# Performance work log

Measured on AMD Instinct MI355X. Metric: run time of the kernel, lower is better.

Reference implementation:

```python
import jax, jax.numpy as jnp
import numpy as np

B, P, D = 256, 256, 514          # batch, num_patches (16^2), model_dim
H, HD = 8, 64                    # n_heads, head_dim ((D-2)//H)
SH = 256                         # shared_hidden = head_mlp_hidden_dims[0]
HH = 256                         # per-head hidden (head_mlp_hidden_dims[1])
DFF = 2048                       # ffn hidden
LH = 2 * SH                      # lat_modulator hidden = shared_hidden*2
LD = D - 2                       # learnable_dim

def gelu(x):
    return jax.nn.gelu(x, approximate=False)  # torch nn.GELU default is exact erf

def setup_inputs() -> dict:
    key = jax.random.key(0)
    ks = jax.random.split(key, 16)
    s = 0.02
    x = jax.random.normal(ks[0], (B, P, D), dtype=jnp.float32)
    # shared spatial layer: Linear(P -> SH), torch weight layout [out, in]
    Ws = jax.random.normal(ks[1], (SH, P), dtype=jnp.float32) * s
    bs = jax.random.normal(ks[2], (SH,), dtype=jnp.float32) * s
    # lat modulator: Linear(2 -> LH), GELU, Linear(LH -> 2*SH) with special init
    LW1 = jax.random.normal(ks[3], (LH, 2), dtype=jnp.float32) * s
    Lb1 = jax.random.normal(ks[4], (LH,), dtype=jnp.float32) * s
    LW2 = jnp.zeros((2 * SH, LH), dtype=jnp.float32)  # zeroed per module init
    Lb2 = jnp.concatenate([jnp.ones((SH,), jnp.float32), jnp.zeros((SH,), jnp.float32)])
    # per-head processing: Linear(SH->HH), GELU, Linear(HH->P), stacked over heads
    HW1 = jax.random.normal(ks[5], (H, HH, SH), dtype=jnp.float32) * s
    Hb1 = jax.random.normal(ks[6], (H, HH), dtype=jnp.float32) * s
    HW2 = jax.random.normal(ks[7], (H, P, HH), dtype=jnp.float32) * s
    Hb2 = jax.random.normal(ks[8], (H, P), dtype=jnp.float32) * s
    # ffn: Linear(D -> DFF) with last-2 input cols zeroed, GELU, Linear(DFF -> LD)
    FW1 = jax.random.normal(ks[9], (DFF, D), dtype=jnp.float32) * s
    FW1 = FW1.at[:, -2:].set(0.0)
    Fb1 = jax.random.normal(ks[10], (DFF,), dtype=jnp.float32) * s
    FW2 = jax.random.normal(ks[11], (LD, DFF), dtype=jnp.float32) * s
    Fb2 = jax.random.normal(ks[12], (LD,), dtype=jnp.float32) * s
    return dict(x=x, Ws=Ws, bs=bs, LW1=LW1, Lb1=Lb1, LW2=LW2, Lb2=Lb2,
                HW1=HW1, Hb1=Hb1, HW2=HW2, Hb2=Hb2,
                FW1=FW1, Fb1=Fb1, FW2=FW2, Fb2=Fb2)

def reference(x, Ws, bs, LW1, Lb1, LW2, Lb2, HW1, Hb1, HW2, Hb2, FW1, Fb1, FW2, Fb2):
    central = P // 2
    sc_central = x[:, central, -2:]          # [B, 2]
    sc_all = x[:, :, -2:]                    # [B, P, 2]
    x_learn = x[:, :, :-2]                   # [B, P, LD]
    x_res = x_learn
    # all heads at once: [B, P, H, HD] -> [B, H, HD, P]
    xh = x_learn.reshape(B, P, H, HD).transpose(0, 2, 3, 1)
    shared = jnp.einsum('bhdp,op->bhdo', xh, Ws) + bs   # [B, H, HD, SH]
    # FiLM params (loop-invariant in original, hoisted here)
    mod = gelu(sc_central @ LW1.T + Lb1) @ LW2.T + Lb2  # [B, 2*SH]
    gamma = mod[:, :SH][:, None, None, :]
    beta = mod[:, SH:][:, None, None, :]
    shared = shared * gamma + beta
    # per-head MLPs as grouped GEMMs
    h = gelu(jnp.einsum('bhdo,hko->bhdk', shared, HW1) + Hb1[None, :, None, :])
    out = jnp.einsum('bhdk,hpk->bhdp', h, HW2) + Hb2[None, :, None, :]  # [B,H,HD,P]
    x_learn = out.transpose(0, 3, 1, 2).reshape(B, P, LD) + x_res
    x_full = jnp.concatenate([x_learn, sc_all], axis=-1)  # [B, P, D]
    f = gelu(x_full @ FW1.T + Fb1) @ FW2.T + Fb2          # [B, P, LD]
    x_learn = f + x_learn
    return jnp.concatenate([x_learn, sc_all], axis=-1)
```

## Files before the change

kernel.cpp:

```cpp
#include <hip/hip_runtime.h>
#include <math.h>

typedef __attribute__((ext_vector_type(8))) __bf16 bf16x8;
typedef __attribute__((ext_vector_type(4))) float f32x4;
typedef __attribute__((ext_vector_type(2))) float f32x2;

#define DEV __device__ __forceinline__

typedef __attribute__((address_space(3))) unsigned int lds_u32;
typedef __attribute__((address_space(1))) unsigned int glb_u32;

DEV unsigned short f2bf(float f) {
    unsigned int u = __builtin_bit_cast(unsigned int, f);
    u += 0x7FFFu + ((u >> 16) & 1u);
    return (unsigned short)(u >> 16);
}
DEV float bf2f(unsigned short u) {
    unsigned int v = (unsigned int)u << 16;
    return __builtin_bit_cast(float, v);
}
DEV unsigned int pack2(float a, float b) {
    return (unsigned int)f2bf(a) | ((unsigned int)f2bf(b) << 16);
}
DEV float gelu_exact(float v) {
    return 0.5f * v * (1.0f + erff(v * 0.70710678118654752f));
}
DEV float gelu_fast(float x) {
    float z = 1.5957691216f * x + 0.0713548163f * x * x * x;
    float e = __expf(-z);
    return x * __builtin_amdgcn_rcpf(1.0f + e);
}

__global__ void cast_bf16_kernel(const float* __restrict__ src,
                                 unsigned short* __restrict__ dst, int n) {
    int i = blockIdx.x * 256 + threadIdx.x;
    if (i < n) dst[i] = f2bf(src[i]);
}

__global__ void cast_fw1_kernel(const float* __restrict__ src,
                                unsigned short* __restrict__ dst) {
    int i = blockIdx.x * 256 + threadIdx.x;
    if (i < 2048 * 512) {
        int row = i >> 9, k = i & 511;
        dst[i] = f2bf(src[row * 514 + k]);
    }
}

__global__ void gb_kernel(const float* __restrict__ x,
                          const float* __restrict__ LW1, const float* __restrict__ Lb1,
                          const float* __restrict__ LW2, const float* __restrict__ Lb2,
                          float* __restrict__ gb) {
    __shared__ float t[8][512];
    const int b0 = blockIdx.x * 8, tid = threadIdx.x;
    for (int idx = tid; idx < 8 * 512; idx += 256) {
        int bb = idx >> 9, j = idx & 511;
        float s0 = x[((size_t)(b0 + bb) * 256 + 128) * 514 + 512];
        float s1 = x[((size_t)(b0 + bb) * 256 + 128) * 514 + 513];
        t[bb][j] = gelu_exact(LW1[j * 2] * s0 + LW1[j * 2 + 1] * s1 + Lb1[j]);
    }
    __syncthreads();
    const int i = tid;
    float a0[8], a1[8];
    float l0 = Lb2[i], l1 = Lb2[i + 256];
    #pragma unroll
    for (int bb = 0; bb < 8; ++bb) { a0[bb] = l0; a1[bb] = l1; }
    for (int j = 0; j < 512; ++j) {
        float w0 = LW2[(size_t)i * 512 + j];
        float w1 = LW2[(size_t)(i + 256) * 512 + j];
        #pragma unroll
        for (int bb = 0; bb < 8; ++bb) {
            a0[bb] += w0 * t[bb][j];
            a1[bb] += w1 * t[bb][j];
        }
    }
    #pragma unroll
    for (int bb = 0; bb < 8; ++bb) {
        gb[(size_t)(b0 + bb) * 512 + i] = a0[bb];
        gb[(size_t)(b0 + bb) * 512 + i + 256] = a1[bb];
    }
}

__global__ void sc_copy_kernel(const float* __restrict__ x, float* __restrict__ out,
                               float* __restrict__ scbuf) {
    size_t idx = (size_t)blockIdx.x * 256 + threadIdx.x;
    size_t off = idx * 514 + 512;
    f32x2 v = *(const f32x2*)(x + off);
    *(f32x2*)(out + off) = v;
    *(f32x2*)(scbuf + idx * 2) = v;
}

#define MPAD 264

__global__ __launch_bounds__(256, 2) void mixer_kernel(
    const float* __restrict__ x, const float* __restrict__ bs,
    const float* __restrict__ Hb1, const float* __restrict__ Hb2,
    const unsigned short* __restrict__ Wsb,
    const unsigned short* __restrict__ HW1b,
    const unsigned short* __restrict__ HW2b,
    const float* __restrict__ gb,
    float* __restrict__ out,
    unsigned short* __restrict__ Xb) {
    __shared__ __attribute__((aligned(16))) char smem[33792 + 34816];
    unsigned short* XT = (unsigned short*)smem;
    unsigned short* S = (unsigned short*)(smem + 33792);
    unsigned short* ST = S;

    const int bid = blockIdx.x;
    const int b = bid >> 3;
    const int h = bid & 7;
    const int tid = threadIdx.x;
    const int lane = tid & 63;
    const int w = tid >> 6;
    const int l15 = lane & 15;
    const int l4 = lane >> 4;

    {
        const int c = lane;
        const float* xp = x + ((size_t)b * 256) * 514 + (size_t)h * 64 + c;
        for (int i = 0; i < 32; ++i) {
            int p = (i * 4 + w) * 2;
            float v0 = xp[(size_t)p * 514];
            float v1 = xp[(size_t)(p + 1) * 514];
            *(unsigned int*)&XT[c * MPAD + p] = pack2(v0, v1);
        }
    }
    __syncthreads();

    f32x4 acc[4][4];

    #pragma unroll
    for (int mt = 0; mt < 4; ++mt)
        #pragma unroll
        for (int nt = 0; nt < 4; ++nt) acc[mt][nt] = 0.f;
    {
        bf16x8 bnx[4];
        #pragma unroll
        for (int nt = 0; nt < 4; ++nt)
            bnx[nt] = *(const bf16x8*)(Wsb + (size_t)(w * 64 + nt * 16 + l15) * 256 + l4 * 8);
        for (int kc = 0; kc < 8; ++kc) {
            bf16x8 bcur[4];
            #pragma unroll
            for (int nt = 0; nt < 4; ++nt) bcur[nt] = bnx[nt];
            if (kc < 7) {
                #pragma unroll
                for (int nt = 0; nt < 4; ++nt)
                    bnx[nt] = *(const bf16x8*)(Wsb + (size_t)(w * 64 + nt * 16 + l15) * 256 + (kc + 1) * 32 + l4 * 8);
            }
            #pragma unroll
            for (int mt = 0; mt < 4; ++mt) {
                bf16x8 afr = *(const bf16x8*)&XT[(mt * 16 + l15) * MPAD + kc * 32 + l4 * 8];
                #pragma unroll
                for (int nt = 0; nt < 4; ++nt)
                    acc[mt][nt] = __builtin_amdgcn_mfma_f32_16x16x32_bf16(afr, bcur[nt], acc[mt][nt], 0, 0, 0);
            }
        }
    }
    #pragma unroll
    for (int nt = 0; nt < 4; ++nt) {
        int o = w * 64 + nt * 16 + l15;
        float bsv = bs[o];
        float g = gb[(size_t)b * 512 + o];
        float be = gb[(size_t)b * 512 + 256 + o];
        #pragma unroll
        for (int mt = 0; mt < 4; ++mt)
            #pragma unroll
            for (int r = 0; r < 4; ++r) {
                int c = mt * 16 + l4 * 4 + r;
                S[c * MPAD + o] = f2bf((acc[mt][nt][r] + bsv) * g + be);
            }
    }
    __syncthreads();

    const unsigned short* W2p = HW1b + (size_t)h * 65536;
    #pragma unroll
    for (int mt = 0; mt < 4; ++mt)
        #pragma unroll
        for (int nt = 0; nt < 4; ++nt) acc[mt][nt] = 0.f;
    {
        bf16x8 bnx[4];
        #pragma unroll
        for (int nt = 0; nt < 4; ++nt)
            bnx[nt] = *(const bf16x8*)(W2p + (size_t)(w * 64 + nt * 16 + l15) * 256 + l4 * 8);
        for (int kc = 0; kc < 8; ++kc) {
            bf16x8 bcur[4];
            #pragma unroll
            for (int nt = 0; nt < 4; ++nt) bcur[nt] = bnx[nt];
            if (kc < 7) {
                #pragma unroll
                for (int nt = 0; nt < 4; ++nt)
                    bnx[nt] = *(const bf16x8*)(W2p + (size_t)(w * 64 + nt * 16 + l15) * 256 + (kc + 1) * 32 + l4 * 8);
            }
            #pragma unroll
            for (int mt = 0; mt < 4; ++mt) {
                bf16x8 afr = *(const bf16x8*)&S[(mt * 16 + l15) * MPAD + kc * 32 + l4 * 8];
                #pragma unroll
                for (int nt = 0; nt < 4; ++nt)
                    acc[mt][nt] = __builtin_amdgcn_mfma_f32_16x16x32_bf16(afr, bcur[nt], acc[mt][nt], 0, 0, 0);
            }
        }
    }
    #pragma unroll
    for (int nt = 0; nt < 4; ++nt) {
        int kk = w * 64 + nt * 16 + l15;
        float hb = Hb1[(size_t)h * 256 + kk];
        #pragma unroll
        for (int mt = 0; mt < 4; ++mt)
            #pragma unroll
            for (int r = 0; r < 4; ++r) {
                int c = mt * 16 + l4 * 4 + r;
                XT[c * MPAD + kk] = f2bf(gelu_fast(acc[mt][nt][r] + hb));
            }
    }
    __syncthreads();

    const unsigned short* W3p = HW2b + (size_t)h * 65536;
    #pragma unroll
    for (int mt = 0; mt < 4; ++mt)
        #pragma unroll
        for (int nt = 0; nt < 4; ++nt) acc[mt][nt] = 0.f;
    {
        bf16x8 bnx[4];
        #pragma unroll
        for (int nt = 0; nt < 4; ++nt)
            bnx[nt] = *(const bf16x8*)(W3p + (size_t)(w * 64 + nt * 16 + l15) * 256 + l4 * 8);
        for (int kc = 0; kc < 8; ++kc) {
            bf16x8 bcur[4];
            #pragma unroll
            for (int nt = 0; nt < 4; ++nt) bcur[nt] = bnx[nt];
            if (kc < 7) {
                #pragma unroll
                for (int nt = 0; nt < 4; ++nt)
                    bnx[nt] = *(const bf16x8*)(W3p + (size_t)(w * 64 + nt * 16 + l15) * 256 + (kc + 1) * 32 + l4 * 8);
            }
            #pragma unroll
            for (int mt = 0; mt < 4; ++mt) {
                bf16x8 afr = *(const bf16x8*)&XT[(mt * 16 + l15) * MPAD + kc * 32 + l4 * 8];
                #pragma unroll
                for (int nt = 0; nt < 4; ++nt)
                    acc[mt][nt] = __builtin_amdgcn_mfma_f32_16x16x32_bf16(afr, bcur[nt], acc[mt][nt], 0, 0, 0);
            }
        }
    }
    #pragma unroll
    for (int nt = 0; nt < 4; ++nt) {
        int p = w * 64 + nt * 16 + l15;
        float hb = Hb2[(size_t)h * 256 + p];
        #pragma unroll
        for (int mt = 0; mt < 4; ++mt) {
            ushort4 uv;
            uv.x = f2bf(acc[mt][nt][0] + hb);
            uv.y = f2bf(acc[mt][nt][1] + hb);
            uv.z = f2bf(acc[mt][nt][2] + hb);
            uv.w = f2bf(acc[mt][nt][3] + hb);
            *(ushort4*)(ST + p * 68 + mt * 16 + l4 * 4) = uv;
        }
    }
    __syncthreads();

    #pragma unroll
    for (int s = 0; s < 16; ++s) {
        int row = s * 16 + w * 4 + l4;
        ushort4 u = *(const ushort4*)(ST + row * 68 + l15 * 4);
        const float* xr = x + ((size_t)(b * 256 + row)) * 514 + h * 64 + l15 * 4;
        f32x2 xa = *(const f32x2*)xr;
        f32x2 xc = *(const f32x2*)(xr + 2);
        float o0 = bf2f(u.x) + xa.x;
        float o1 = bf2f(u.y) + xa.y;
        float o2 = bf2f(u.z) + xc.x;
        float o3 = bf2f(u.w) + xc.y;
        float* orow = out + ((size_t)(b * 256 + row)) * 514 + h * 64 + l15 * 4;
        f32x2 w0; w0.x = o0; w0.y = o1;
        f32x2 w1; w1.x = o2; w1.y = o3;
        *(f32x2*)orow = w0;
        *(f32x2*)(orow + 2) = w1;
        ushort4 xo;
        xo.x = f2bf(o0); xo.y = f2bf(o1); xo.z = f2bf(o2); xo.w = f2bf(o3);
        *(ushort4*)(Xb + ((size_t)(b * 256 + row)) * 512 + h * 64 + l15 * 4) = xo;
    }
}

DEV void stage_half(const unsigned short* g, size_t gstride, int row0, int k0,
                    char* half_base, int w, int lane) {
    const int slot = lane & 7;
    const int r8 = lane >> 3;
    const int swz = (slot ^ r8) * 16;
    #pragma unroll
    for (int i = 0; i < 2; ++i) {
        int chunk = w * 2 + i;
        int row = chunk * 8 + r8;
        const char* src = (const char*)(g + (size_t)(row0 + row) * gstride + k0) + swz;
        __builtin_amdgcn_global_load_lds((const glb_u32*)src,
                                         (lds_u32*)(half_base + chunk * 1024), 16, 0, 0);
    }
}

DEV void stage4(const unsigned short* A, size_t sA, int m0,
                const unsigned short* B, size_t sB, int n0, int k0,
                char* Abuf, char* Bbuf, int w, int lane) {
    stage_half(A, sA, m0, k0, Abuf, w, lane);
    stage_half(A, sA, m0 + 128, k0, Abuf + 16384, w, lane);
    stage_half(B, sB, n0, k0, Bbuf, w, lane);
    stage_half(B, sB, n0 + 128, k0, Bbuf + 16384, w, lane);
}

DEV void tile_body(const unsigned short* A, size_t sA, int m0,
                   const unsigned short* B, size_t sB, int n0,
                   char* smem, int cb, int kn, bool more,
                   int vA0, int vA1, int vB0, int vB1,
                   int w, int lane, f32x4 (&acc)[8][4]) {
    if (more) {
        int nb = 32768 - cb;
        stage4(A, sA, m0, B, sB, n0, kn, smem + nb, smem + 65536 + nb, w, lane);
    }
    __builtin_amdgcn_s_setprio(1);
    #pragma unroll
    for (int kk = 0; kk < 2; ++kk) {
        const int vA = kk ? vA1 : vA0;
        const int vB = kk ? vB1 : vB0;
        bf16x8 bf[4];
        #pragma unroll
        for (int nf = 0; nf < 4; ++nf)
            bf[nf] = *(const bf16x8*)(smem + vB + cb + nf * 2048);
        #pragma unroll
        for (int mh = 0; mh < 2; ++mh) {
            bf16x8 af[4];
            #pragma unroll
            for (int mf = 0; mf < 4; ++mf)
                af[mf] = *(const bf16x8*)(smem + vA + cb + mh * 8192 + mf * 2048);
            #pragma unroll
            for (int mf = 0; mf < 4; ++mf)
                #pragma unroll
                for (int nf = 0; nf < 4; ++nf)
                    acc[mh * 4 + mf][nf] = __builtin_amdgcn_mfma_f32_16x16x32_bf16(
                        af[mf], bf[nf], acc[mh * 4 + mf][nf], 0, 0, 0);
        }
    }
    __builtin_amdgcn_s_setprio(0);
    if (more) asm volatile("s_waitcnt vmcnt(0)" ::: "memory");
    __builtin_amdgcn_s_barrier();
}

DEV void gemm_loop(const unsigned short* A, size_t sA,
                   const unsigned short* B, size_t sB,
                   int m0, int n0, int NT,
                   char* smem, int w, int lane, f32x4 (&acc)[8][4]) {
    const int wm = w >> 2, wn = w & 3;
    const int l15 = lane & 15, l4 = lane >> 4;
    const int sw = (l15 & 7) << 4;
    const int k0off = (l4 * 16) ^ sw;
    const int k1off = (64 + l4 * 16) ^ sw;
    const int aBase = (wm * 128 + l15) * 128;
    const int bBase = 65536 + (wn * 64 + l15) * 128;
    const int vA0 = aBase + k0off, vA1 = aBase + k1off;
    const int vB0 = bBase + k0off, vB1 = bBase + k1off;

    stage4(A, sA, m0, B, sB, n0, 0, smem, smem + 65536, w, lane);
    asm volatile("s_waitcnt vmcnt(0)" ::: "memory");
    __builtin_amdgcn_s_barrier();

    for (int t = 0; t < NT; t += 2) {
        tile_body(A, sA, m0, B, sB, n0, smem, 0, (t + 1) * 64, t + 1 < NT,
                  vA0, vA1, vB0, vB1, w, lane, acc);
        tile_body(A, sA, m0, B, sB, n0, smem, 32768, (t + 2) * 64, t + 2 < NT,
                  vA0, vA1, vB0, vB1, w, lane, acc);
    }
}

__global__ __launch_bounds__(512, 1) void gemm1_kernel(
    const unsigned short* __restrict__ A,
    const unsigned short* __restrict__ B,
    const float* __restrict__ Fb1,
    const float* __restrict__ FW1,
    const float* __restrict__ scbuf,
    long pass_m0,
    unsigned short* __restrict__ G) {
    __shared__ __attribute__((aligned(16))) char smem[131072];

    const int nwg = gridDim.x;
    const int cpx = nwg >> 3;
    const int bid = (blockIdx.x & 7) * cpx + (blockIdx.x >> 3);
    const int m0 = (bid >> 3) * 256;
    const int n0 = (bid & 7) * 256;
    const int tid = threadIdx.x;
    const int lane = tid & 63;
    const int w = tid >> 6;
    const int l15 = lane & 15;
    const int l4 = lane >> 4;
    const int wm = w >> 2, wn = w & 3;

    f32x4 acc[8][4];
    #pragma unroll
    for (int mf = 0; mf < 8; ++mf)
        #pragma unroll
        for (int nf = 0; nf < 4; ++nf) acc[mf][nf] = 0.f;

    gemm_loop(A, 512, B, 512, m0, n0, 8, smem, w, lane, acc);

    float fb[4], wa[4], wb[4];
    #pragma unroll
    for (int nf = 0; nf < 4; ++nf) {
        int n = n0 + wn * 64 + nf * 16 + l15;
        fb[nf] = Fb1[n];
        wa[nf] = FW1[(size_t)n * 514 + 512];
        wb[nf] = FW1[(size_t)n * 514 + 513];
    }
    unsigned short* LT = (unsigned short*)smem;
    #pragma unroll
    for (int ph = 0; ph < 2; ++ph) {
        if (wm == ph) {
            #pragma unroll
            for (int mfg = 0; mfg < 8; ++mfg) {
                f32x2 sc[4];
                #pragma unroll
                for (int r = 0; r < 4; ++r) {
                    long rowg = pass_m0 + m0 + ph * 128 + mfg * 16 + l4 * 4 + r;
                    sc[r] = *(const f32x2*)(scbuf + rowg * 2);
                }
                #pragma unroll
                for (int nf = 0; nf < 4; ++nf)
                    #pragma unroll
                    for (int r = 0; r < 4; ++r) {
                        float v = acc[mfg][nf][r] + fb[nf] + sc[r].x * wa[nf] + sc[r].y * wb[nf];
                        int rl = mfg * 16 + l4 * 4 + r;
                        LT[rl * 264 + wn * 64 + nf * 16 + l15] = f2bf(gelu_fast(v));
                    }
            }
        }
        __syncthreads();
        {
            const int row16 = tid >> 5, col16 = tid & 31;
            #pragma unroll
            for (int sp = 0; sp < 8; ++sp) {
                int row = sp * 16 + row16;
                uint4 d = *(const uint4*)((const char*)smem + row * 528 + col16 * 16);
                *(uint4*)(G + ((size_t)(m0 + ph * 128 + row)) * 2048 + n0 + col16 * 8) = d;
            }
        }
        __syncthreads();
    }
}

__global__ __launch_bounds__(512, 1) void gemm2_kernel(
    const unsigned short* __restrict__ A,
    const unsigned short* __restrict__ B,
    const float* __restrict__ Fb2,
    long pass_m0,
    float* __restrict__ io) {
    __shared__ __attribute__((aligned(16))) char smem[131072];

    const int nwg = gridDim.x;
    const int cpx = nwg >> 3;
    const int bid = (blockIdx.x & 7) * cpx + (blockIdx.x >> 3);
    const int m0 = (bid >> 1) * 256;
    const int n0 = (bid & 1) * 256;
    const int tid = threadIdx.x;
    const int lane = tid & 63;
    const int w = tid >> 6;
    const int l15 = lane & 15;
    const int l4 = lane >> 4;
    const int wm = w >> 2, wn = w & 3;

    f32x4 acc[8][4];
    #pragma unroll
    for (int mf = 0; mf < 8; ++mf)
        #pragma unroll
        for (int nf = 0; nf < 4; ++nf) acc[mf][nf] = 0.f;

    gemm_loop(A, 2048, B, 2048, m0, n0, 32, smem, w, lane, acc);

    #pragma unroll
    for (int nf = 0; nf < 4; ++nf) {
        int n = n0 + wn * 64 + nf * 16 + l15;
        float fbv = Fb2[n];
        #pragma unroll
        for (int mfg = 0; mfg < 8; ++mfg)
            #pragma unroll
            for (int r = 0; r < 4; ++r) {
                long rowg = pass_m0 + m0 + wm * 128 + mfg * 16 + l4 * 4 + r;
                float* p = io + rowg * 514 + n;
                *p = acc[mfg][nf][r] + fbv + *p;
            }
    }
}

extern "C" void kernel_launch(void* const* d_in, const int* in_sizes, int n_in,
                              void* d_out, int out_size, void* d_ws, size_t ws_size,
                              hipStream_t stream) {
    const float* x = (const float*)d_in[0];
    const float* Ws = (const float*)d_in[1];
    const float* bs = (const float*)d_in[2];
    const float* LW1 = (const float*)d_in[3];
    const float* Lb1 = (const float*)d_in[4];
    const float* LW2 = (const float*)d_in[5];
    const float* Lb2 = (const float*)d_in[6];
    const float* HW1 = (const float*)d_in[7];
    const float* Hb1 = (const float*)d_in[8];
    const float* HW2 = (const float*)d_in[9];
    const float* Hb2 = (const float*)d_in[10];
    const float* FW1 = (const float*)d_in[11];
    const float* Fb1 = (const float*)d_in[12];
    const float* FW2 = (const float*)d_in[13];
    const float* Fb2 = (const float*)d_in[14];
    float* out = (float*)d_out;

    char* ws = (char*)d_ws;
    unsigned short* Wsb = (unsigned short*)(ws);
    unsigned short* HW1b = (unsigned short*)(ws + 131072);
    unsigned short* HW2b = (unsigned short*)(ws + 1179648);
    unsigned short* FW1b = (unsigned short*)(ws + 2228224);
    unsigned short* FW2b = (unsigned short*)(ws + 4325376);
    float* gb = (float*)(ws + 6422528);
    float* scbuf = (float*)(ws + 6946816);
    unsigned short* Xb = (unsigned short*)(ws + 7471104);
    unsigned short* Gbuf = (unsigned short*)(ws + 7471104 + 67108864);

    const size_t fixed = 7471104 + 67108864;
    int npass = 32;
    for (int np = 2; np <= 32; np *= 2) {
        if (fixed + (size_t)268435456 / np <= ws_size) { npass = np; break; }
    }
    const long Mtot = 65536;
    const long Mp = Mtot / npass;

    cast_bf16_kernel<<<256, 256, 0, stream>>>(Ws, Wsb, 65536);
    cast_bf16_kernel<<<2048, 256, 0, stream>>>(HW1, HW1b, 524288);
    cast_bf16_kernel<<<2048, 256, 0, stream>>>(HW2, HW2b, 524288);
    cast_bf16_kernel<<<4096, 256, 0, stream>>>(FW2, FW2b, 1048576);
    cast_fw1_kernel<<<4096, 256, 0, stream>>>(FW1, FW1b);
    gb_kernel<<<32, 256, 0, stream>>>(x, LW1, Lb1, LW2, Lb2, gb);
    sc_copy_kernel<<<256, 256, 0, stream>>>(x, out, scbuf);

    mixer_kernel<<<2048, 256, 0, stream>>>(x, bs, Hb1, Hb2, Wsb, HW1b, HW2b, gb, out, Xb);

    for (int p = 0; p < npass; ++p) {
        long m0 = (long)p * Mp;
        gemm1_kernel<<<(int)(Mp / 256) * 8, 512, 0, stream>>>(
            Xb + m0 * 512, FW1b, Fb1, FW1, scbuf, m0, Gbuf);
        gemm2_kernel<<<(int)(Mp / 256) * 2, 512, 0, stream>>>(
            Gbuf, FW2b, Fb2, m0, out);
    }
}
```

Measured before the change: 714.7 us.

## Keep mixer residual in LDS and source FFN residual from bf16 Xb

The mixer kernel now takes its residual from the bf16 transposed x tile already staged in LDS, so it no longer re-reads x from global memory. It also stops writing the fp32 intermediate to the output and writes only the bf16 Xb. gemm2 then takes its residual from Xb and overwrites the output, where it used to read-modify-write the fp32 output. This removes a large fp32 store and two fp32 reads, but the residual path is now held in bf16 and loses precision, and two extra barriers are added so the reused LDS regions are not overwritten early.

```diff
diff --git a/kernel.cpp b/kernel.cpp
--- a/kernel.cpp
+++ b/kernel.cpp
@@ -98,7 +98,6 @@
     const unsigned short* __restrict__ HW1b,
     const unsigned short* __restrict__ HW2b,
     const float* __restrict__ gb,
-    float* __restrict__ out,
     unsigned short* __restrict__ Xb) {
     __shared__ __attribute__((aligned(16))) char smem[33792 + 34816];
     unsigned short* XT = (unsigned short*)smem;
@@ -199,6 +198,7 @@
             }
         }
     }
+    __syncthreads();
     #pragma unroll
     for (int nt = 0; nt < 4; ++nt) {
         int kk = w * 64 + nt * 16 + l15;
@@ -208,7 +208,7 @@
             #pragma unroll
             for (int r = 0; r < 4; ++r) {
                 int c = mt * 16 + l4 * 4 + r;
-                XT[c * MPAD + kk] = f2bf(gelu_fast(acc[mt][nt][r] + hb));
+                S[c * MPAD + kk] = f2bf(gelu_fast(acc[mt][nt][r] + hb));
             }
     }
     __syncthreads();
@@ -234,25 +234,28 @@
             }
             #pragma unroll
             for (int mt = 0; mt < 4; ++mt) {
-                bf16x8 afr = *(const bf16x8*)&XT[(mt * 16 + l15) * MPAD + kc * 32 + l4 * 8];
+                bf16x8 afr = *(const bf16x8*)&S[(mt * 16 + l15) * MPAD + kc * 32 + l4 * 8];
                 #pragma unroll
                 for (int nt = 0; nt < 4; ++nt)
                     acc[mt][nt] = __builtin_amdgcn_mfma_f32_16x16x32_bf16(afr, bcur[nt], acc[mt][nt], 0, 0, 0);
             }
         }
     }
+    __syncthreads();
+
     #pragma unroll
     for (int nt = 0; nt < 4; ++nt) {
         int p = w * 64 + nt * 16 + l15;
         float hb = Hb2[(size_t)h * 256 + p];
         #pragma unroll
         for (int mt = 0; mt < 4; ++mt) {
+            int c0 = mt * 16 + l4 * 4;
             ushort4 uv;
-            uv.x = f2bf(acc[mt][nt][0] + hb);
-            uv.y = f2bf(acc[mt][nt][1] + hb);
-            uv.z = f2bf(acc[mt][nt][2] + hb);
-            uv.w = f2bf(acc[mt][nt][3] + hb);
-            *(ushort4*)(ST + p * 68 + mt * 16 + l4 * 4) = uv;
+            uv.x = f2bf(acc[mt][nt][0] + hb + bf2f(XT[(c0 + 0) * MPAD + p]));
+            uv.y = f2bf(acc[mt][nt][1] + hb + bf2f(XT[(c0 + 1) * MPAD + p]));
+            uv.z = f2bf(acc[mt][nt][2] + hb + bf2f(XT[(c0 + 2) * MPAD + p]));
+            uv.w = f2bf(acc[mt][nt][3] + hb + bf2f(XT[(c0 + 3) * MPAD + p]));
+            *(ushort4*)(ST + p * 68 + c0) = uv;
         }
     }
     __syncthreads();
@@ -261,21 +264,7 @@
     for (int s = 0; s < 16; ++s) {
         int row = s * 16 + w * 4 + l4;
         ushort4 u = *(const ushort4*)(ST + row * 68 + l15 * 4);
-        const float* xr = x + ((size_t)(b * 256 + row)) * 514 + h * 64 + l15 * 4;
-        f32x2 xa = *(const f32x2*)xr;
-        f32x2 xc = *(const f32x2*)(xr + 2);
-        float o0 = bf2f(u.x) + xa.x;
-        float o1 = bf2f(u.y) + xa.y;
-        float o2 = bf2f(u.z) + xc.x;
-        float o3 = bf2f(u.w) + xc.y;
-        float* orow = out + ((size_t)(b * 256 + row)) * 514 + h * 64 + l15 * 4;
-        f32x2 w0; w0.x = o0; w0.y = o1;
-        f32x2 w1; w1.x = o2; w1.y = o3;
-        *(f32x2*)orow = w0;
-        *(f32x2*)(orow + 2) = w1;
-        ushort4 xo;
-        xo.x = f2bf(o0); xo.y = f2bf(o1); xo.z = f2bf(o2); xo.w = f2bf(o3);
-        *(ushort4*)(Xb + ((size_t)(b * 256 + row)) * 512 + h * 64 + l15 * 4) = xo;
+        *(ushort4*)(Xb + ((size_t)(b * 256 + row)) * 512 + h * 64 + l15 * 4) = u;
     }
 }
 
@@ -444,6 +433,7 @@
     const unsigned short* __restrict__ A,
     const unsigned short* __restrict__ B,
     const float* __restrict__ Fb2,
+    const unsigned short* __restrict__ Xb,
     long pass_m0,
     float* __restrict__ io) {
     __shared__ __attribute__((aligned(16))) char smem[131072];
@@ -477,8 +467,8 @@
             #pragma unroll
             for (int r = 0; r < 4; ++r) {
                 long rowg = pass_m0 + m0 + wm * 128 + mfg * 16 + l4 * 4 + r;
-                float* p = io + rowg * 514 + n;
-                *p = acc[mfg][nf][r] + fbv + *p;
+                float resv = bf2f(Xb[(size_t)rowg * 512 + n]);
+                io[rowg * 514 + n] = acc[mfg][nf][r] + fbv + resv;
             }
     }
 }
@@ -530,13 +520,13 @@
     gb_kernel<<<32, 256, 0, stream>>>(x, LW1, Lb1, LW2, Lb2, gb);
     sc_copy_kernel<<<256, 256, 0, stream>>>(x, out, scbuf);
 
-    mixer_kernel<<<2048, 256, 0, stream>>>(x, bs, Hb1, Hb2, Wsb, HW1b, HW2b, gb, out, Xb);
+    mixer_kernel<<<2048, 256, 0, stream>>>(x, bs, Hb1, Hb2, Wsb, HW1b, HW2b, gb, Xb);
 
     for (int p = 0; p < npass; ++p) {
         long m0 = (long)p * Mp;
         gemm1_kernel<<<(int)(Mp / 256) * 8, 512, 0, stream>>>(
             Xb + m0 * 512, FW1b, Fb1, FW1, scbuf, m0, Gbuf);
         gemm2_kernel<<<(int)(Mp / 256) * 2, 512, 0, stream>>>(
-            Gbuf, FW2b, Fb2, m0, out);
-    }
-}
+            Gbuf, FW2b, Fb2, Xb, m0, out);
+    }
+}
```

Measured after the change: 665.8 us. 6.8% less time.
